# Performance work log

Measured on AMD Instinct MI355X. Metric: run time of the kernel, lower is better.

## Reference

```python
import jax, jax.numpy as jnp
import numpy as np

B = 2_000_000
CLAMP_MIN = 0.01
NORM_EPS = 1e-5


def setup_inputs() -> dict:
    key = jax.random.key(0)
    F = jax.random.normal(key, (B, 3, 3), dtype=jnp.float32)
    # learned scalar parameters (per init_kwargs)
    youngs_modulus_log = jnp.asarray(13.0, dtype=jnp.float32)
    poissons_ratio = jnp.asarray(0.3, dtype=jnp.float32)
    yield_stress = jnp.asarray(3000.0, dtype=jnp.float32)
    return {
        "F": F,
        "youngs_modulus_log": youngs_modulus_log,
        "poissons_ratio": poissons_ratio,
        "yield_stress": yield_stress,
    }


def reference(F, youngs_modulus_log, poissons_ratio, yield_stress):
    # von-Mises return mapping on singular values of the deformation gradient
    youngs_modulus = jnp.exp(youngs_modulus_log)
    mu = youngs_modulus / (2.0 * (1.0 + poissons_ratio))  # shear modulus

    # batched 3x3 SVD: U (B,3,3), sigma (B,3), Vh (B,3,3)
    U, sigma, Vh = jnp.linalg.svd(F, full_matrices=False)

    sigma = jnp.maximum(sigma, CLAMP_MIN)
    epsilon = jnp.log(sigma)                                  # (B,3) Hencky strain
    epsilon_trace = jnp.sum(epsilon, axis=1, keepdims=True)   # (B,1)
    epsilon_bar = epsilon - epsilon_trace / 3.0               # deviatoric strain
    epsilon_bar_norm = jnp.linalg.norm(epsilon_bar, axis=1, keepdims=True) + NORM_EPS

    delta_gamma = epsilon_bar_norm - yield_stress / (2.0 * mu)  # (B,1)
    yield_epsilon = epsilon - (delta_gamma / epsilon_bar_norm) * epsilon_bar
    yield_sigma = jnp.exp(yield_epsilon)

    sigma = jnp.where(delta_gamma > 0.0, yield_sigma, sigma)  # (B,3)

    # F_corrected = U @ diag(sigma) @ Vh, fused without materializing diag
    F_corrected = jnp.einsum("bij,bj,bjk->bik", U, sigma, Vh)
    return F_corrected
```

## Files before the change

kernel.cpp:

```cpp
#include <hip/hip_runtime.h>
#include <math.h>

#define TPB 64
#define NQ 2
#define CHUNK (TPB * NQ)
#define CH_F (CHUNK * 9)
#define CH_F4 (CH_F / 4)

typedef float v2  __attribute__((ext_vector_type(2)));
typedef int   v2i __attribute__((ext_vector_type(2)));

static __device__ __forceinline__ v2 V2(float x){ v2 r; r.x=x; r.y=x; return r; }
static __device__ __forceinline__ v2 vfma(v2 a, v2 b, v2 c){ return __builtin_elementwise_fma(a, b, c); }
static __device__ __forceinline__ v2 vmax(v2 a, v2 b){ return __builtin_elementwise_max(a, b); }
static __device__ __forceinline__ v2 vabs(v2 a){ return __builtin_elementwise_abs(a); }
static __device__ __forceinline__ v2 vcps(v2 a, v2 b){ return __builtin_elementwise_copysign(a, b); }

static __device__ __forceinline__ v2 rsq2(v2 x){ v2 r; r.x=__builtin_amdgcn_rsqf(x.x);  r.y=__builtin_amdgcn_rsqf(x.y);  return r; }
static __device__ __forceinline__ v2 rcp2(v2 x){ v2 r; r.x=__builtin_amdgcn_rcpf(x.x);  r.y=__builtin_amdgcn_rcpf(x.y);  return r; }
static __device__ __forceinline__ v2 sqt2(v2 x){ v2 r; r.x=__builtin_amdgcn_sqrtf(x.x); r.y=__builtin_amdgcn_sqrtf(x.y); return r; }
static __device__ __forceinline__ v2 lg22(v2 x){ v2 r; r.x=__builtin_amdgcn_logf(x.x);  r.y=__builtin_amdgcn_logf(x.y);  return r; }
static __device__ __forceinline__ v2 ex22(v2 x){ v2 r; r.x=__builtin_amdgcn_exp2f(x.x); r.y=__builtin_amdgcn_exp2f(x.y); return r; }

static __device__ __forceinline__ v2 vsel(v2i m, v2 a, v2 b){
  v2i ai = __builtin_bit_cast(v2i, a), bi = __builtin_bit_cast(v2i, b);
  return __builtin_bit_cast(v2, bi ^ ((ai ^ bi) & m));
}

static __device__ __forceinline__ void gl_lds16(const float* g, float* l){
  __builtin_amdgcn_global_load_lds(
      (const __attribute__((address_space(1))) void*)g,
      (__attribute__((address_space(3))) void*)l, 16, 0, 0);
}

static __device__ __forceinline__ void lds_fence(){
  asm volatile("s_waitcnt lgkmcnt(0)" ::: "memory");
  __builtin_amdgcn_sched_barrier(0);
}

__device__ __forceinline__ void jcs2(v2 app_in, v2 aqq_in, v2 apq,
                                     v2& c, v2& s,
                                     v2& app_out, v2& aqq_out)
{
  v2 d    = (aqq_in - app_in) * 0.5f;
  v2 r2   = vmax(vfma(d, d, apq * apq), V2(1e-30f));
  v2 invh = rsq2(r2);
  v2 h    = r2 * invh;
  v2 sg   = vcps(V2(1.0f), d);
  v2 ch   = h + vabs(d);
  v2 sh   = apq * sg;
  v2 w    = rsq2(vfma(ch, ch, sh * sh));
  c = ch * w;
  s = sh * w;
  v2 hs = h * sg;
  v2 m  = app_in + d;
  app_out = m - hs;
  aqq_out = m + hs;
}

__device__ __forceinline__ void jrot(v2& app, v2& aqq, v2& apq,
                                     v2& apk, v2& aqk,
                                     v2& vp0, v2& vp1, v2& vp2,
                                     v2& vq0, v2& vq1, v2& vq2)
{
  v2 c, s;
  jcs2(app, aqq, apq, c, s, app, aqq);
  apq = V2(0.0f);
  v2 pk = apk, qk = aqk;
  apk = c * pk - s * qk;
  aqk = s * pk + c * qk;
  v2 v;
  v = vp0; vp0 = c*v - s*vq0; vq0 = s*v + c*vq0;
  v = vp1; vp1 = c*v - s*vq1; vq1 = s*v + c*vq1;
  v = vp2; vp2 = c*v - s*vq2; vq2 = s*v + c*vq2;
}

#define CSWAP(li, lj, a0, a1, a2, b0, b1, b2)                                   \
  do {                                                                          \
    v2i _m = (li) < (lj);                                                       \
    v2 _t;                                                                      \
    _t = vsel(_m,(lj),(li)); (lj) = vsel(_m,(li),(lj)); (li) = _t;              \
    _t = vsel(_m,(b0),(a0)); (b0) = vsel(_m,(a0),(b0)); (a0) = _t;              \
    _t = vsel(_m,(b1),(a1)); (b1) = vsel(_m,(a1),(b1)); (a1) = _t;              \
    _t = vsel(_m,(b2),(a2)); (b2) = vsel(_m,(a2),(b2)); (a2) = _t;              \
  } while (0)

__global__ __launch_bounds__(TPB) void plastic_svd_kernel(
    const float* __restrict__ F,
    const float* __restrict__ p_yml,
    const float* __restrict__ p_nu,
    const float* __restrict__ p_ys,
    float* __restrict__ out,
    int nmat, int nchunks)
{
  __shared__ float lds[2][CH_F];
  const int tid = threadIdx.x;

  const float mu_s = __builtin_amdgcn_exp2f(p_yml[0] * 1.44269504f) *
                     __builtin_amdgcn_rcpf(2.0f * (1.0f + p_nu[0]));
  const float qy_s = p_ys[0] * 0.5f * __builtin_amdgcn_rcpf(mu_s);
  const v2 qy = V2(qy_s);

  auto STAGE = [&](int t, int b){
    const int fbase = t * CH_F;
    const int rem = nmat - t * CHUNK;
    const int nfl = (rem >= CHUNK ? CHUNK : rem) * 9;
    const int nfl4 = nfl >> 2;
    const float4* g4 = (const float4*)(F + fbase);
    #pragma unroll
    for (int k = 0; k < 5; ++k) {
      int i4 = k * TPB + tid;
      if (i4 < CH_F4 && i4 < nfl4)
        gl_lds16((const float*)(g4 + i4), &lds[b][i4 * 4]);
    }
    int i = (nfl & ~3) + tid;
    if (i < nfl) lds[b][i] = F[fbase + i];
    for (int i2 = nfl + tid; i2 < CH_F; i2 += TPB) lds[b][i2] = 0.0f;
  };

  int cur = 0;
  const int t0 = blockIdx.x;
  if (t0 < nchunks) STAGE(t0, 0);

  for (int t = t0; t < nchunks; t += gridDim.x) {
    __syncthreads();
    const int tn = t + gridDim.x;
    if (tn < nchunks) STAGE(tn, cur ^ 1);

    const int blockBase = t * CHUNK;
    const int gbase = blockBase * 9;
    const int mi0 = blockBase + tid;
    const int mi1 = blockBase + TPB + tid;
    float* bufc = lds[cur];
    const float* mA = &bufc[tid * 9];
    const float* mB = &bufc[(TPB + tid) * 9];

    v2 s00, s11, s22, s01, s02, s12;
    {
      v2 f00,f01,f02,f10,f11,f12,f20,f21,f22;
      f00.x=mA[0]; f01.x=mA[1]; f02.x=mA[2];
      f10.x=mA[3]; f11.x=mA[4]; f12.x=mA[5];
      f20.x=mA[6]; f21.x=mA[7]; f22.x=mA[8];
      f00.y=mB[0]; f01.y=mB[1]; f02.y=mB[2];
      f10.y=mB[3]; f11.y=mB[4]; f12.y=mB[5];
      f20.y=mB[6]; f21.y=mB[7]; f22.y=mB[8];
      s00 = f00*f00 + f10*f10 + f20*f20;
      s11 = f01*f01 + f11*f11 + f21*f21;
      s22 = f02*f02 + f12*f12 + f22*f22;
      s01 = f00*f01 + f10*f11 + f20*f21;
      s02 = f00*f02 + f10*f12 + f20*f22;
      s12 = f01*f02 + f11*f12 + f21*f22;
    }

    v2 v00,v01,v02,v10,v11,v12,v20,v21,v22;
    v2 c, s;

    jcs2(s00, s11, s01, c, s, s00, s11);
    { v2 pk = s02, qk = s12; s02 = c*pk - s*qk; s12 = s*pk + c*qk; }
    v00 = c;  v01 = s;
    v10 = -s; v11 = c;
    s01 = V2(0.0f);
    jcs2(s00, s22, s02, c, s, s00, s22);
    { v2 pk = s01, qk = s12; s01 = c*pk - s*qk; s12 = s*pk + c*qk; }
    v02 = s * v00; v12 = s * v10; v22 = c;
    v00 = c * v00; v10 = c * v10; v20 = -s;
    v21 = V2(0.0f);
    s02 = V2(0.0f);
    jrot(s11, s22, s12, s01, s02, v01, v11, v21, v02, v12, v22);
    jrot(s00, s11, s01, s02, s12, v00, v10, v20, v01, v11, v21);
    jrot(s00, s22, s02, s01, s12, v00, v10, v20, v02, v12, v22);
    jrot(s11, s22, s12, s01, s02, v01, v11, v21, v02, v12, v22);
    jrot(s00, s11, s01, s02, s12, v00, v10, v20, v01, v11, v21);
    jrot(s00, s22, s02, s01, s12, v00, v10, v20, v02, v12, v22);
    jcs2(s11, s22, s12, c, s, s11, s22);
    { v2 v;
      v = v01; v01 = c*v - s*v02; v02 = s*v + c*v02;
      v = v11; v11 = c*v - s*v12; v12 = s*v + c*v12;
      v = v21; v21 = c*v - s*v22; v22 = s*v + c*v22; }

    v2 l0 = s00, l1 = s11, l2 = s22;
    CSWAP(l0, l1, v00, v10, v20, v01, v11, v21);
    CSWAP(l1, l2, v01, v11, v21, v02, v12, v22);
    CSWAP(l0, l1, v00, v10, v20, v01, v11, v21);

    v2 f00,f01,f02,f10,f11,f12,f20,f21,f22;
    f00.x=mA[0]; f01.x=mA[1]; f02.x=mA[2];
    f10.x=mA[3]; f11.x=mA[4]; f12.x=mA[5];
    f20.x=mA[6]; f21.x=mA[7]; f22.x=mA[8];
    f00.y=mB[0]; f01.y=mB[1]; f02.y=mB[2];
    f10.y=mB[3]; f11.y=mB[4]; f12.y=mB[5];
    f20.y=mB[6]; f21.y=mB[7]; f22.y=mB[8];

    v2 w0x = f00*v00 + f01*v10 + f02*v20;
    v2 w0y = f10*v00 + f11*v10 + f12*v20;
    v2 w0z = f20*v00 + f21*v10 + f22*v20;
    v2 n0sq = w0x*w0x + w0y*w0y + w0z*w0z;
    v2 inv0 = rsq2(vmax(n0sq, V2(1e-30f)));
    v2 u0x = w0x*inv0, u0y = w0y*inv0, u0z = w0z*inv0;

    v2 w1x = f00*v01 + f01*v11 + f02*v21;
    v2 w1y = f10*v01 + f11*v11 + f12*v21;
    v2 w1z = f20*v01 + f21*v11 + f22*v21;
    v2 n1sq_pre = w1x*w1x + w1y*w1y + w1z*w1z;
    v2 d01 = w1x*u0x + w1y*u0y + w1z*u0z;
    w1x = w1x - d01*u0x; w1y = w1y - d01*u0y; w1z = w1z - d01*u0z;
    v2 n1sq = w1x*w1x + w1y*w1y + w1z*w1z;
    v2 inv1 = rsq2(vmax(n1sq, V2(1e-30f)));
    v2 u1x = w1x*inv1, u1y = w1y*inv1, u1z = w1z*inv1;

    v2 u2x = u0y*u1z - u0z*u1y;
    v2 u2y = u0z*u1x - u0x*u1z;
    v2 u2z = u0x*u1y - u0y*u1x;
    v2 w2x = f00*v02 + f01*v12 + f02*v22;
    v2 w2y = f10*v02 + f11*v12 + f12*v22;
    v2 w2z = f20*v02 + f21*v12 + f22*v22;
    v2 s2d = u2x*w2x + u2y*w2y + u2z*w2z;
    v2 sg = vcps(V2(1.0f), s2d);
    v2 sig2 = vabs(s2d);
    u2x = u2x * sg; u2y = u2y * sg; u2z = u2z * sg;

    v2 e0 = lg22(vmax(n0sq,     V2(1e-4f))) * 0.5f;
    v2 e1 = lg22(vmax(n1sq_pre, V2(1e-4f))) * 0.5f;
    v2 e2 = lg22(vmax(sig2,     V2(0.01f)));
    v2 m3 = (e0 + e1 + e2) * (1.0f / 3.0f);
    v2 b0 = e0 - m3, b1 = e1 - m3, b2 = e2 - m3;
    v2 bn = sqt2(b0*b0 + b1*b1 + b2*b2) * 0.69314718f + V2(1e-5f);
    v2 r = vmax(bn - qy, V2(0.0f)) * rcp2(bn);
    v2 c0 = ex22(e0 - r * b0);
    v2 c1 = ex22(e1 - r * b1);
    v2 c2 = ex22(e2 - r * b2);

    v2 a0x = c0*u0x, a0y = c0*u0y, a0z = c0*u0z;
    v2 a1x = c1*u1x, a1y = c1*u1y, a1z = c1*u1z;
    v2 a2x = c2*u2x, a2y = c2*u2y, a2z = c2*u2z;

    v2 o00 = a0x*v00 + a1x*v01 + a2x*v02;
    v2 o01 = a0x*v10 + a1x*v11 + a2x*v12;
    v2 o02 = a0x*v20 + a1x*v21 + a2x*v22;
    v2 o10 = a0y*v00 + a1y*v01 + a2y*v02;
    v2 o11 = a0y*v10 + a1y*v11 + a2y*v12;
    v2 o12 = a0y*v20 + a1y*v21 + a2y*v22;
    v2 o20 = a0z*v00 + a1z*v01 + a2z*v02;
    v2 o21 = a0z*v10 + a1z*v11 + a2z*v12;
    v2 o22 = a0z*v20 + a1z*v21 + a2z*v22;

    if (mi0 < nmat) {
      float* m = &bufc[tid * 9];
      m[0]=o00.x; m[1]=o01.x; m[2]=o02.x;
      m[3]=o10.x; m[4]=o11.x; m[5]=o12.x;
      m[6]=o20.x; m[7]=o21.x; m[8]=o22.x;
    }
    if (mi1 < nmat) {
      float* m = &bufc[(TPB + tid) * 9];
      m[0]=o00.y; m[1]=o01.y; m[2]=o02.y;
      m[3]=o10.y; m[4]=o11.y; m[5]=o12.y;
      m[6]=o20.y; m[7]=o21.y; m[8]=o22.y;
    }
    lds_fence();

    {
      const int rem = nmat - blockBase;
      const int nfl = (rem >= CHUNK ? CHUNK : rem) * 9;
      const int nfl4 = nfl >> 2;
      float4* g4 = (float4*)(out + gbase);
      const float4* l4 = (const float4*)bufc;
      #pragma unroll
      for (int k = 0; k < 5; ++k) {
        int i4 = k * TPB + tid;
        if (i4 < CH_F4 && i4 < nfl4) g4[i4] = l4[i4];
      }
      int i = (nfl & ~3) + tid;
      if (i < nfl) out[gbase + i] = bufc[i];
    }
    cur ^= 1;
  }
}

extern "C" void kernel_launch(void* const* d_in, const int* in_sizes, int n_in,
                              void* d_out, int out_size, void* d_ws, size_t ws_size,
                              hipStream_t stream) {
  const float* F     = (const float*)d_in[0];
  const float* p_yml = (const float*)d_in[1];
  const float* p_nu  = (const float*)d_in[2];
  const float* p_ys  = (const float*)d_in[3];
  float* out = (float*)d_out;

  const int nmat = in_sizes[0] / 9;
  const int nchunks = (nmat + CHUNK - 1) / CHUNK;
  int G = 16 * 256;
  if (G > nchunks) G = nchunks;
  hipLaunchKernelGGL(plastic_svd_kernel, dim3(G), dim3(TPB), 0, stream,
                     F, p_yml, p_nu, p_ys, out, nmat, nchunks);
}
```

Measured before the change: 35.92 us.

## Replace block barrier with vmcnt waits and keep F in registers

Drops the per-iteration __syncthreads and instead uses s_waitcnt vmcnt so each wave waits only for its own older global-to-LDS loads. STAGE now clamps addresses so it always issues a fixed number of loads, which lets the vmcnt count be predictable. F is kept in registers across the SVD instead of being re-read from LDS. Removing the barrier assumes each thread only touches LDS data it loaded itself, which holds with one wave per block but is fragile. STAGE is now also called unconditionally, even for blocks with no work.

```diff
diff --git a/kernel.cpp b/kernel.cpp
--- a/kernel.cpp
+++ b/kernel.cpp
@@ -6,6 +6,7 @@
 #define CHUNK (TPB * NQ)
 #define CH_F (CHUNK * 9)
 #define CH_F4 (CH_F / 4)
+#define NSTG 5
 
 typedef float v2  __attribute__((ext_vector_type(2)));
 typedef int   v2i __attribute__((ext_vector_type(2)));
@@ -31,11 +32,6 @@
   __builtin_amdgcn_global_load_lds(
       (const __attribute__((address_space(1))) void*)g,
       (__attribute__((address_space(3))) void*)l, 16, 0, 0);
-}
-
-static __device__ __forceinline__ void lds_fence(){
-  asm volatile("s_waitcnt lgkmcnt(0)" ::: "memory");
-  __builtin_amdgcn_sched_barrier(0);
 }
 
 __device__ __forceinline__ void jcs2(v2 app_in, v2 aqq_in, v2 apq,
@@ -95,6 +91,8 @@
 {
   __shared__ float lds[2][CH_F];
   const int tid = threadIdx.x;
+  const int totF  = nmat * 9;
+  const int totF4 = totF >> 2;
 
   const float mu_s = __builtin_amdgcn_exp2f(p_yml[0] * 1.44269504f) *
                      __builtin_amdgcn_rcpf(2.0f * (1.0f + p_nu[0]));
@@ -102,30 +100,36 @@
   const v2 qy = V2(qy_s);
 
   auto STAGE = [&](int t, int b){
-    const int fbase = t * CH_F;
-    const int rem = nmat - t * CHUNK;
-    const int nfl = (rem >= CHUNK ? CHUNK : rem) * 9;
-    const int nfl4 = nfl >> 2;
-    const float4* g4 = (const float4*)(F + fbase);
+    const int f4base = t * CH_F4;
     #pragma unroll
     for (int k = 0; k < 5; ++k) {
       int i4 = k * TPB + tid;
-      if (i4 < CH_F4 && i4 < nfl4)
-        gl_lds16((const float*)(g4 + i4), &lds[b][i4 * 4]);
-    }
-    int i = (nfl & ~3) + tid;
-    if (i < nfl) lds[b][i] = F[fbase + i];
-    for (int i2 = nfl + tid; i2 < CH_F; i2 += TPB) lds[b][i2] = 0.0f;
+      if (i4 < CH_F4) {
+        int gi4 = f4base + i4;
+        gi4 = gi4 < totF4 ? gi4 : totF4 - 1;
+        gl_lds16((const float*)((const float4*)F + gi4), &lds[b][i4 * 4]);
+      }
+    }
+    if ((totF & 3) && t == nchunks - 1) {
+      int e = (totF & ~3) + tid;
+      if (e < totF) lds[b][e - t * CH_F] = F[e];
+    }
   };
 
   int cur = 0;
   const int t0 = blockIdx.x;
-  if (t0 < nchunks) STAGE(t0, 0);
+  STAGE(t0, 0);
 
   for (int t = t0; t < nchunks; t += gridDim.x) {
-    __syncthreads();
     const int tn = t + gridDim.x;
-    if (tn < nchunks) STAGE(tn, cur ^ 1);
+    const bool pf = tn < nchunks;
+    if (pf) {
+      STAGE(tn, cur ^ 1);
+      asm volatile("s_waitcnt vmcnt(5)" ::: "memory");
+    } else {
+      asm volatile("s_waitcnt vmcnt(0)" ::: "memory");
+    }
+    __builtin_amdgcn_sched_barrier(0);
 
     const int blockBase = t * CHUNK;
     const int gbase = blockBase * 9;
@@ -135,22 +139,20 @@
     const float* mA = &bufc[tid * 9];
     const float* mB = &bufc[(TPB + tid) * 9];
 
-    v2 s00, s11, s22, s01, s02, s12;
-    {
-      v2 f00,f01,f02,f10,f11,f12,f20,f21,f22;
-      f00.x=mA[0]; f01.x=mA[1]; f02.x=mA[2];
-      f10.x=mA[3]; f11.x=mA[4]; f12.x=mA[5];
-      f20.x=mA[6]; f21.x=mA[7]; f22.x=mA[8];
-      f00.y=mB[0]; f01.y=mB[1]; f02.y=mB[2];
-      f10.y=mB[3]; f11.y=mB[4]; f12.y=mB[5];
-      f20.y=mB[6]; f21.y=mB[7]; f22.y=mB[8];
-      s00 = f00*f00 + f10*f10 + f20*f20;
-      s11 = f01*f01 + f11*f11 + f21*f21;
-      s22 = f02*f02 + f12*f12 + f22*f22;
-      s01 = f00*f01 + f10*f11 + f20*f21;
-      s02 = f00*f02 + f10*f12 + f20*f22;
-      s12 = f01*f02 + f11*f12 + f21*f22;
-    }
+    v2 f00,f01,f02,f10,f11,f12,f20,f21,f22;
+    f00.x=mA[0]; f01.x=mA[1]; f02.x=mA[2];
+    f10.x=mA[3]; f11.x=mA[4]; f12.x=mA[5];
+    f20.x=mA[6]; f21.x=mA[7]; f22.x=mA[8];
+    f00.y=mB[0]; f01.y=mB[1]; f02.y=mB[2];
+    f10.y=mB[3]; f11.y=mB[4]; f12.y=mB[5];
+    f20.y=mB[6]; f21.y=mB[7]; f22.y=mB[8];
+
+    v2 s00 = f00*f00 + f10*f10 + f20*f20;
+    v2 s11 = f01*f01 + f11*f11 + f21*f21;
+    v2 s22 = f02*f02 + f12*f12 + f22*f22;
+    v2 s01 = f00*f01 + f10*f11 + f20*f21;
+    v2 s02 = f00*f02 + f10*f12 + f20*f22;
+    v2 s12 = f01*f02 + f11*f12 + f21*f22;
 
     v2 v00,v01,v02,v10,v11,v12,v20,v21,v22;
     v2 c, s;
@@ -183,14 +185,6 @@
     CSWAP(l1, l2, v01, v11, v21, v02, v12, v22);
     CSWAP(l0, l1, v00, v10, v20, v01, v11, v21);
 
-    v2 f00,f01,f02,f10,f11,f12,f20,f21,f22;
-    f00.x=mA[0]; f01.x=mA[1]; f02.x=mA[2];
-    f10.x=mA[3]; f11.x=mA[4]; f12.x=mA[5];
-    f20.x=mA[6]; f21.x=mA[7]; f22.x=mA[8];
-    f00.y=mB[0]; f01.y=mB[1]; f02.y=mB[2];
-    f10.y=mB[3]; f11.y=mB[4]; f12.y=mB[5];
-    f20.y=mB[6]; f21.y=mB[7]; f22.y=mB[8];
-
     v2 w0x = f00*v00 + f01*v10 + f02*v20;
     v2 w0y = f10*v00 + f11*v10 + f12*v20;
     v2 w0z = f20*v00 + f21*v10 + f22*v20;
@@ -256,7 +250,8 @@
       m[3]=o10.y; m[4]=o11.y; m[5]=o12.y;
       m[6]=o20.y; m[7]=o21.y; m[8]=o22.y;
     }
-    lds_fence();
+    asm volatile("s_waitcnt lgkmcnt(0)" ::: "memory");
+    __builtin_amdgcn_sched_barrier(0);
 
     {
       const int rem = nmat - blockBase;
```

Result: no change. 36.28 us (+1.0%).
